# Kernel optimization log

Hardware: AMD Instinct MI355X
Metric: run time of the kernel (lower is better)

The kernel has to match this reference:

```python
import jax, jax.numpy as jnp
import numpy as np

N, C, H = 100000, 128, 8
D = C // H  # 16
E = 1600000
EPS = 1e-5
NEG_SLOPE = 0.2


def layer_norm(x, g, b):
    mu = jnp.mean(x, axis=-1, keepdims=True)
    var = jnp.mean(jnp.square(x - mu), axis=-1, keepdims=True)
    return (x - mu) * jax.lax.rsqrt(var + EPS) * g + b


def setup_inputs() -> dict:
    key = jax.random.key(0)
    ks = jax.random.split(key, 16)
    s = lambda fan: 1.0 / np.sqrt(fan)
    return {
        "x0": jax.random.normal(ks[0], (N, C), jnp.float32),
        "edges": jax.random.randint(ks[1], (2, E), 0, N, jnp.int64) if jax.config.jax_enable_x64 else jax.random.randint(ks[1], (2, E), 0, N, jnp.int32),
        "lin_l_w": jax.random.normal(ks[2], (C, C), jnp.float32) * s(C),
        "lin_r_w": jax.random.normal(ks[3], (C, C), jnp.float32) * s(C),
        "att": jax.random.normal(ks[4], (H, D), jnp.float32) * s(D),
        "gat_bias": jnp.zeros((C,), jnp.float32),
        "W_w": jax.random.normal(ks[5], (C, C), jnp.float32) * s(C),
        "g1": jnp.ones((C,), jnp.float32),
        "b1": jnp.zeros((C,), jnp.float32),
        "mlp_w1": jax.random.normal(ks[6], (2 * C, C), jnp.float32) * s(C),
        "mlp_b1": jnp.zeros((2 * C,), jnp.float32),
        "mlp_w2": jax.random.normal(ks[7], (C, 2 * C), jnp.float32) * s(2 * C),
        "mlp_b2": jnp.zeros((C,), jnp.float32),
        "g2": jnp.ones((C,), jnp.float32),
        "b2": jnp.zeros((C,), jnp.float32),
    }


def gatv2(x, edges, lin_l_w, lin_r_w, att, gat_bias):
    # GATv2Conv (concat=True, negative_slope=0.2, eval mode: no dropout)
    src, dst = edges[0], edges[1]
    x_l = (x @ lin_l_w.T).reshape(N, H, D)  # source transform
    x_r = (x @ lin_r_w.T).reshape(N, H, D)  # target transform
    e = jax.nn.leaky_relu(x_l[src] + x_r[dst], NEG_SLOPE)  # [E,H,D]
    logits = jnp.einsum("ehd,hd->eh", e, att)  # [E,H]
    # segment softmax over incoming edges per target node
    m = jax.ops.segment_max(logits, dst, num_segments=N)  # [N,H]
    m = jnp.where(jnp.isfinite(m), m, 0.0)
    ex = jnp.exp(logits - m[dst])
    denom = jax.ops.segment_sum(ex, dst, num_segments=N)  # [N,H]
    alpha = ex / (denom[dst] + 1e-16)  # [E,H]
    out = jax.ops.segment_sum(alpha[:, :, None] * x_l[src], dst, num_segments=N)
    return out.reshape(N, C) + gat_bias


def reference(x0, edges, lin_l_w, lin_r_w, att, gat_bias, W_w, g1, b1,
              mlp_w1, mlp_b1, mlp_w2, mlp_b2, g2, b2):
    x1 = gatv2(x0, edges, lin_l_w, lin_r_w, att, gat_bias)
    x2 = x1 @ W_w.T + x0
    x3 = layer_norm(x2, g1, b1)
    h = jax.nn.relu(x3 @ mlp_w1.T + mlp_b1)
    x4 = h @ mlp_w2.T + mlp_b2 + x3
    return layer_norm(x4, g2, b2)
```

## Files before the change

kernel.cpp:

```cpp
#include <hip/hip_runtime.h>

#define NN 100000
#define CC 128
#define HHEADS 8
#define EE 1600000
#define NB 196
#define BCAP 10240
#define BSTRIDE 16
#define P1C 3125

typedef unsigned short u16;
typedef unsigned int u32;
typedef __attribute__((ext_vector_type(8))) u16 u16x8;
typedef __attribute__((ext_vector_type(4))) u16 u16x4;
typedef __attribute__((ext_vector_type(8))) __bf16 bf16x8;
typedef __attribute__((ext_vector_type(4))) float f32x4;
typedef __attribute__((ext_vector_type(2))) float f32x2;

__device__ __forceinline__ float bf2f(u16 u) {
    union { u32 i; float f; } v; v.i = ((u32)u) << 16; return v.f;
}
__device__ __forceinline__ u16 f2bf(float f) {
    union { float f; u32 i; } v; v.f = f;
    u32 r = v.i + 0x7FFFu + ((v.i >> 16) & 1u);
    return (u16)(r >> 16);
}
__device__ __forceinline__ float fexp2(float x) {
    float r;
    asm volatile("v_exp_f32 %0, %1" : "=v"(r) : "v"(x));
    return r;
}

__device__ __forceinline__ f32x4 mfma16(u16x8 a, u16x8 b, f32x4 c) {
    return __builtin_amdgcn_mfma_f32_16x16x32_bf16(
        __builtin_bit_cast(bf16x8, a), __builtin_bit_cast(bf16x8, b), c, 0, 0, 0);
}

#define GLOAD(gp, lp) __builtin_amdgcn_global_load_lds( \
    (const __attribute__((address_space(1))) u32*)(gp), \
    (__attribute__((address_space(3))) u32*)(lp), 16, 0, 0)

__global__ __launch_bounds__(256) void k_pre(
    const int* __restrict__ src, const int* __restrict__ dst,
    int* __restrict__ bucketCnt, u32* __restrict__ bucketEdges,
    const float* __restrict__ x0, u16* __restrict__ x0b,
    const float* __restrict__ s0, const float* __restrict__ s1,
    const float* __restrict__ s2, const float* __restrict__ s3,
    const float* __restrict__ s4,
    u16* __restrict__ d0, u16* __restrict__ d1, u16* __restrict__ d2,
    u16* __restrict__ d3, u16* __restrict__ d4)
{
    const int b = blockIdx.x, tid = threadIdx.x;
    if (b < 512) {
        __shared__ u32 s_src[P1C];
        __shared__ u32 s_dst[P1C];
        __shared__ u32 hist[256], ssum[256], bstart[256], base[256], seq[256];
        const int beg = b * P1C;

        hist[tid] = 0; seq[tid] = 0;
        __syncthreads();

        int es[13], ds[13];
#pragma unroll
        for (int j = 0; j < 13; j++) {
            int o = tid + j * 256;
            if (o < P1C) { es[j] = src[beg + o]; ds[j] = dst[beg + o]; }
            else { es[j] = -1; ds[j] = 0; }
        }
#pragma unroll
        for (int j = 0; j < 13; j++)
            if (es[j] >= 0) atomicAdd(&hist[(u32)ds[j] >> 9], 1u);
        __syncthreads();

        u32 h = hist[tid];
        ssum[tid] = h;
        __syncthreads();
        for (int o = 1; o < 256; o <<= 1) {
            u32 v = ssum[tid];
            u32 a = (tid >= o) ? ssum[tid - o] : 0;
            __syncthreads();
            ssum[tid] = v + a;
            __syncthreads();
        }
        bstart[tid] = ssum[tid] - h;
        if (tid < NB) base[tid] = h ? (u32)atomicAdd(&bucketCnt[tid * BSTRIDE], (int)h) : 0u;
        __syncthreads();

#pragma unroll
        for (int j = 0; j < 13; j++) {
            if (es[j] >= 0) {
                u32 bb = (u32)ds[j] >> 9;
                u32 r = atomicAdd(&seq[bb], 1u);
                u32 pos = bstart[bb] + r;
                s_src[pos] = (u32)es[j];
                s_dst[pos] = (u32)ds[j];
            }
        }
        __syncthreads();

        for (int i = tid; i < P1C; i += 256) {
            u32 d = s_dst[i];
            u32 bb = d >> 9;
            u32 go = base[bb] + ((u32)i - bstart[bb]);
            if (go < BCAP)
                bucketEdges[(size_t)bb * BCAP + go] = s_src[i] | ((d & 511u) << 17);
        }
    } else if (b < 2560) {
        const int n = NN * CC;
        const int stride = 2048 * 256 * 4;
        for (int i = ((b - 512) * 256 + tid) * 4; i < n; i += stride) {
            float4 v = *(const float4*)(x0 + i);
            u16x4 o;
            o.x = f2bf(v.x); o.y = f2bf(v.y); o.z = f2bf(v.z); o.w = f2bf(v.w);
            *(u16x4*)(x0b + i) = o;
        }
    } else {
        int wb = b - 2560;
        const float* s; u16* d; int boff;
        if (wb < 16)      { s = s0; d = d0; boff = wb; }
        else if (wb < 32) { s = s1; d = d1; boff = wb - 16; }
        else if (wb < 48) { s = s2; d = d2; boff = wb - 32; }
        else if (wb < 80) { s = s3; d = d3; boff = wb - 48; }
        else              { s = s4; d = d4; boff = wb - 80; }
        int i = boff * 1024 + tid * 4;
        float4 v = *(const float4*)(s + i);
        u16x4 o;
        o.x = f2bf(v.x); o.y = f2bf(v.y); o.z = f2bf(v.z); o.w = f2bf(v.w);
        *(u16x4*)(d + i) = o;
    }
}

__global__ __launch_bounds__(256) void k_p2(const int* __restrict__ bucketCnt,
                                            u32* __restrict__ bucketEdges,
                                            int* __restrict__ offs,
                                            int* __restrict__ cnt)
{
    __shared__ u32 ebuf[BCAP];
    __shared__ u32 ncnt[512], loff[512], ssum[256];
    const int b = blockIdx.x, tid = threadIdx.x;
    int n = bucketCnt[b * BSTRIDE]; n = n < BCAP ? n : BCAP;
    u32* be = bucketEdges + (size_t)b * BCAP;

    for (int i = tid; i < n; i += 256) ebuf[i] = be[i];
    ncnt[tid] = 0; ncnt[tid + 256] = 0;
    __syncthreads();
    for (int i = tid; i < n; i += 256) atomicAdd(&ncnt[(ebuf[i] >> 17) & 511], 1u);
    __syncthreads();

    u32 a0 = ncnt[2 * tid], a1 = ncnt[2 * tid + 1];
    ssum[tid] = a0 + a1;
    __syncthreads();
    for (int o = 1; o < 256; o <<= 1) {
        u32 v = ssum[tid];
        u32 add = (tid >= o) ? ssum[tid - o] : 0;
        __syncthreads();
        ssum[tid] = v + add;
        __syncthreads();
    }
    u32 excl = ssum[tid] - (a0 + a1);
    loff[2 * tid] = excl;
    loff[2 * tid + 1] = excl + a0;

    int node0 = b * 512 + 2 * tid;
    if (node0 < NN)     { offs[node0]     = b * BCAP + (int)excl;            cnt[node0]     = (int)a0; }
    if (node0 + 1 < NN) { offs[node0 + 1] = b * BCAP + (int)(excl + a0);     cnt[node0 + 1] = (int)a1; }

    ncnt[tid] = 0; ncnt[tid + 256] = 0;
    __syncthreads();
    for (int i = tid; i < n; i += 256) {
        u32 e = ebuf[i];
        u32 ln = (e >> 17) & 511;
        u32 r = atomicAdd(&ncnt[ln], 1u);
        be[loff[ln] + r] = e & 0x1FFFFu;
    }
}

template<int K, bool BIAS, bool RELU, bool RESIDB, bool LNF>
__global__ __launch_bounds__(256, 4) void k_gemm(
    const u16* __restrict__ A, const u16* __restrict__ B,
    const float* __restrict__ bias, const u16* __restrict__ residb,
    const float* __restrict__ g, const float* __restrict__ bln,
    float* __restrict__ outf, u16* __restrict__ outb, int M, int NC)
{
    __shared__ __align__(16) u16 As[128 * 64];
    __shared__ __align__(16) u16 Bs[128 * 64];
    __shared__ float lsum[2][128], lsq[2][128];

    const int tid = threadIdx.x;
    const int lane = tid & 63;
    const int w = tid >> 6;
    const int wr = w >> 1, wc = w & 1;
    const int row0 = blockIdx.x * 128;
    const int col0 = blockIdx.y * 128;
    f32x4 acc[4][4] = {};

    for (int kt = 0; kt < K; kt += 64) {
#pragma unroll
        for (int i = 0; i < 4; i++) {
            int c = i * 256 + tid;
            int r = c >> 3;
            int kc = (c & 7) * 8;
            int ar = row0 + r; ar = ar < M ? ar : M - 1;
            GLOAD(A + (size_t)ar * K + kt + kc, As + r * 64 + kc);
            GLOAD(B + (size_t)(col0 + r) * K + kt + kc, Bs + r * 64 + kc);
        }
        asm volatile("s_waitcnt vmcnt(0)" ::: "memory");
        __syncthreads();
#pragma unroll
        for (int kk = 0; kk < 2; kk++) {
            const int ko = kk * 32 + (lane >> 4) * 8;
            u16x8 af[4], bfr[4];
#pragma unroll
            for (int m = 0; m < 4; m++)
                af[m] = *(const u16x8*)(As + (wr * 64 + m * 16 + (lane & 15)) * 64 + ko);
#pragma unroll
            for (int n = 0; n < 4; n++)
                bfr[n] = *(const u16x8*)(Bs + (wc * 64 + n * 16 + (lane & 15)) * 64 + ko);
#pragma unroll
            for (int m = 0; m < 4; m++)
#pragma unroll
                for (int n = 0; n < 4; n++)
                    acc[m][n] = mfma16(af[m], bfr[n], acc[m][n]);
        }
        __syncthreads();
    }

    const int rbase = wr * 64 + ((lane >> 4) << 2);
    const int cbase = wc * 64 + (lane & 15);

    if constexpr (!LNF) {
#pragma unroll
        for (int m = 0; m < 4; m++) {
#pragma unroll
            for (int j = 0; j < 4; j++) {
                int gr = row0 + rbase + m * 16 + j;
                if (gr < M) {
                    size_t rowoff = (size_t)gr * NC;
#pragma unroll
                    for (int n = 0; n < 4; n++) {
                        int gc = col0 + cbase + n * 16;
                        float v = acc[m][n][j];
                        if constexpr (BIAS)  v += bias[gc];
                        if constexpr (RELU)  v = fmaxf(v, 0.f);
                        if (outf) outf[rowoff + gc] = v;
                        if (outb) outb[rowoff + gc] = f2bf(v);
                    }
                }
            }
        }
    } else {
        float gv[4], bv[4];
#pragma unroll
        for (int n = 0; n < 4; n++) { gv[n] = g[cbase + n * 16]; bv[n] = bln[cbase + n * 16]; }
#pragma unroll
        for (int m = 0; m < 4; m++) {
#pragma unroll
            for (int j = 0; j < 4; j++) {
                int lr = rbase + m * 16 + j;
                int gr = row0 + lr; gr = gr < M ? gr : M - 1;
                float s = 0.f, q = 0.f;
#pragma unroll
                for (int n = 0; n < 4; n++) {
                    float v = acc[m][n][j];
                    if constexpr (BIAS)   v += bias[cbase + n * 16];
                    if constexpr (RESIDB) v += bf2f(residb[(size_t)gr * 128 + cbase + n * 16]);
                    if constexpr (RELU)   v = fmaxf(v, 0.f);
                    acc[m][n][j] = v;
                    s += v; q += v * v;
                }
                s += __shfl_xor(s, 1, 16); q += __shfl_xor(q, 1, 16);
                s += __shfl_xor(s, 2, 16); q += __shfl_xor(q, 2, 16);
                s += __shfl_xor(s, 4, 16); q += __shfl_xor(q, 4, 16);
                s += __shfl_xor(s, 8, 16); q += __shfl_xor(q, 8, 16);
                if ((lane & 15) == 0) { lsum[wc][lr] = s; lsq[wc][lr] = q; }
            }
        }
        __syncthreads();
#pragma unroll
        for (int m = 0; m < 4; m++) {
#pragma unroll
            for (int j = 0; j < 4; j++) {
                int lr = rbase + m * 16 + j;
                int gr = row0 + lr;
                if (gr < M) {
                    float s = lsum[0][lr] + lsum[1][lr];
                    float q = lsq[0][lr] + lsq[1][lr];
                    float mu = s * (1.f / 128.f);
                    float var = q * (1.f / 128.f) - mu * mu;
                    float rs = rsqrtf(var + 1e-5f);
                    size_t rowoff = (size_t)gr * 128;
#pragma unroll
                    for (int n = 0; n < 4; n++) {
                        float y = fmaf((acc[m][n][j] - mu) * rs, gv[n], bv[n]);
                        int gc = cbase + n * 16;
                        if (outf) outf[rowoff + gc] = y;
                        if (outb) outb[rowoff + gc] = f2bf(y);
                    }
                }
            }
        }
    }
}

__global__ __launch_bounds__(256, 2) void k_mlp(
    const u16* __restrict__ x3b, const u16* __restrict__ W1,
    const float* __restrict__ mb1, const u16* __restrict__ W2,
    const float* __restrict__ mb2, const float* __restrict__ g2,
    const float* __restrict__ b2, float* __restrict__ out, int M)
{
    __shared__ __align__(16) u16 x3s[128 * 128];
    __shared__ __align__(16) u16 hs[128 * 130];
    __shared__ float lsum[2][128], lsq[2][128];

    const int tid = threadIdx.x;
    const int lane = tid & 63;
    const int w = tid >> 6;
    const int wr = w >> 1, wc = w & 1;
    const int row0 = blockIdx.x * 128;
    const int rbase = wr * 64 + ((lane >> 4) << 2);
    const int cbase = wc * 64 + (lane & 15);

#pragma unroll
    for (int i = 0; i < 8; i++) {
        int c = i * 256 + tid;
        int r = c >> 4;
        int kc = (c & 15) * 8;
        int ar = row0 + r; ar = ar < M ? ar : M - 1;
        GLOAD(x3b + (size_t)ar * 128 + kc, x3s + r * 128 + kc);
    }
    asm volatile("s_waitcnt vmcnt(0)" ::: "memory");
    __syncthreads();

    f32x4 accB[4][4] = {};
    for (int half = 0; half < 2; half++) {
        f32x4 accA[4][4] = {};
#pragma unroll
        for (int kk = 0; kk < 4; kk++) {
            const int ko = kk * 32 + (lane >> 4) * 8;
            u16x8 af[4], bfr[4];
#pragma unroll
            for (int m = 0; m < 4; m++)
                af[m] = *(const u16x8*)(x3s + (wr * 64 + m * 16 + (lane & 15)) * 128 + ko);
#pragma unroll
            for (int n = 0; n < 4; n++)
                bfr[n] = *(const u16x8*)(W1 + (size_t)(half * 128 + wc * 64 + n * 16 + (lane & 15)) * 128 + ko);
#pragma unroll
            for (int m = 0; m < 4; m++)
#pragma unroll
                for (int n = 0; n < 4; n++)
                    accA[m][n] = mfma16(af[m], bfr[n], accA[m][n]);
        }
        float bv[4];
#pragma unroll
        for (int n = 0; n < 4; n++) bv[n] = mb1[half * 128 + cbase + n * 16];
#pragma unroll
        for (int m = 0; m < 4; m++)
#pragma unroll
            for (int n = 0; n < 4; n++) {
                int lc = cbase + n * 16;
#pragma unroll
                for (int j = 0; j < 4; j++) {
                    float v = fmaxf(accA[m][n][j] + bv[n], 0.f);
                    hs[(rbase + m * 16 + j) * 130 + lc] = f2bf(v);
                }
            }
        __syncthreads();

#pragma unroll
        for (int kk = 0; kk < 4; kk++) {
            const int ko = kk * 32 + (lane >> 4) * 8;
            u16x8 af[4], bfr[4];
#pragma unroll
            for (int m = 0; m < 4; m++)
                af[m] = *(const u16x8*)(hs + (wr * 64 + m * 16 + (lane & 15)) * 130 + ko);
#pragma unroll
            for (int n = 0; n < 4; n++)
                bfr[n] = *(const u16x8*)(W2 + (size_t)(wc * 64 + n * 16 + (lane & 15)) * 256 + half * 128 + ko);
#pragma unroll
            for (int m = 0; m < 4; m++)
#pragma unroll
                for (int n = 0; n < 4; n++)
                    accB[m][n] = mfma16(af[m], bfr[n], accB[m][n]);
        }
        __syncthreads();
    }

    float gv[4], bvln[4], bv2[4];
#pragma unroll
    for (int n = 0; n < 4; n++) {
        gv[n] = g2[cbase + n * 16];
        bvln[n] = b2[cbase + n * 16];
        bv2[n] = mb2[cbase + n * 16];
    }
#pragma unroll
    for (int m = 0; m < 4; m++) {
#pragma unroll
        for (int j = 0; j < 4; j++) {
            int lr = rbase + m * 16 + j;
            float s = 0.f, q = 0.f;
#pragma unroll
            for (int n = 0; n < 4; n++) {
                float v = accB[m][n][j] + bv2[n] + bf2f(x3s[lr * 128 + cbase + n * 16]);
                accB[m][n][j] = v;
                s += v; q += v * v;
            }
            s += __shfl_xor(s, 1, 16); q += __shfl_xor(q, 1, 16);
            s += __shfl_xor(s, 2, 16); q += __shfl_xor(q, 2, 16);
            s += __shfl_xor(s, 4, 16); q += __shfl_xor(q, 4, 16);
            s += __shfl_xor(s, 8, 16); q += __shfl_xor(q, 8, 16);
            if ((lane & 15) == 0) { lsum[wc][lr] = s; lsq[wc][lr] = q; }
        }
    }
    __syncthreads();
#pragma unroll
    for (int m = 0; m < 4; m++) {
#pragma unroll
        for (int j = 0; j < 4; j++) {
            int lr = rbase + m * 16 + j;
            int gr = row0 + lr;
            if (gr < M) {
                float s = lsum[0][lr] + lsum[1][lr];
                float q = lsq[0][lr] + lsq[1][lr];
                float mu = s * (1.f / 128.f);
                float var = q * (1.f / 128.f) - mu * mu;
                float rs = rsqrtf(var + 1e-5f);
                size_t rowoff = (size_t)gr * 128;
#pragma unroll
                for (int n = 0; n < 4; n++)
                    out[rowoff + cbase + n * 16] =
                        fmaf((accB[m][n][j] - mu) * rs, gv[n], bvln[n]);
            }
        }
    }
}

__global__ __launch_bounds__(256) void k_gat(const u16* __restrict__ xlr,
                                             const u32* __restrict__ csr,
                                             const int* __restrict__ offs,
                                             const int* __restrict__ cnt,
                                             const float* __restrict__ att,
                                             const float* __restrict__ gbias,
                                             u16* __restrict__ x1b)
{
    const int node = blockIdx.x * 4 + (threadIdx.x >> 6);
    const int lane = threadIdx.x & 63;
    const int slot = lane >> 4;
    const int sub  = lane & 15;
    const int c0   = sub * 8;
    const float L2E = 1.44269504f;

    f32x4 alo = *(const f32x4*)(att + c0);
    f32x4 ahi = *(const f32x4*)(att + c0 + 4);
    f32x2 av[4];
    av[0] = f32x2{alo[0], alo[1]} * L2E; av[1] = f32x2{alo[2], alo[3]} * L2E;
    av[2] = f32x2{ahi[0], ahi[1]} * L2E; av[3] = f32x2{ahi[2], ahi[3]} * L2E;

    u16x8 xr8 = *(const u16x8*)(xlr + (size_t)node * 256 + 128 + c0);
    f32x2 xrv[4];
#pragma unroll
    for (int j = 0; j < 4; j++) xrv[j] = f32x2{bf2f(xr8[2 * j]), bf2f(xr8[2 * j + 1])};

    const int beg = offs[node];
    const int deg = cnt[node];
    const int ng = (deg + 3) >> 2;

    float s = 0.f;
    f32x2 accv[4] = {};

    u16x8 xgA = {}, xgB = {};
    int ixC = 0;
    if (deg > 0) {
        int dm1 = deg - 1;
        int e0 = slot      < dm1 ? slot      : dm1;
        int e1 = slot + 4  < dm1 ? slot + 4  : dm1;
        int e2 = slot + 8  < dm1 ? slot + 8  : dm1;
        int i0 = (int)csr[beg + e0];
        int i1 = (int)csr[beg + e1];
        ixC    = (int)csr[beg + e2];
        xgA = *(const u16x8*)(xlr + (size_t)i0 * 256 + c0);
        xgB = *(const u16x8*)(xlr + (size_t)i1 * 256 + c0);
    }

    for (int g = 0; g < ng; g++) {
        u16x8 cur = xgA;
        xgA = xgB;
        xgB = *(const u16x8*)(xlr + (size_t)ixC * 256 + c0);
        int en = 4 * (g + 3) + slot; en = en < deg - 1 ? en : deg - 1;
        ixC = (int)csr[beg + (en > 0 ? en : 0)];

        const int e = 4 * g + slot;
        f32x2 xlv[4];
        f32x2 dot = {0.f, 0.f};
#pragma unroll
        for (int j = 0; j < 4; j++) {
            f32x2 xl = f32x2{bf2f(cur[2 * j]), bf2f(cur[2 * j + 1])};
            xlv[j] = xl;
            f32x2 t = xl + xrv[j];
            f32x2 t2 = t * 0.2f;
            f32x2 lr = f32x2{fmaxf(t.x, t2.x), fmaxf(t.y, t2.y)};
            dot += av[j] * lr;
        }
        float p = dot.x + dot.y;
        p += __shfl_xor(p, 1);
        float wgt = (e < deg) ? fexp2(p) : 0.f;
        s += wgt;
#pragma unroll
        for (int j = 0; j < 4; j++) accv[j] += xlv[j] * wgt;
    }

    s += __shfl_xor(s, 16);
    s += __shfl_xor(s, 32);
#pragma unroll
    for (int j = 0; j < 4; j++) {
        accv[j].x += __shfl_xor(accv[j].x, 16);
        accv[j].y += __shfl_xor(accv[j].y, 16);
        accv[j].x += __shfl_xor(accv[j].x, 32);
        accv[j].y += __shfl_xor(accv[j].y, 32);
    }

    if (slot == 0) {
        float inv = 1.f / (s + 1e-16f);
        u16x8 o;
#pragma unroll
        for (int j = 0; j < 4; j++) {
            o[2 * j]     = f2bf(fmaf(accv[j].x, inv, gbias[c0 + 2 * j]));
            o[2 * j + 1] = f2bf(fmaf(accv[j].y, inv, gbias[c0 + 2 * j + 1]));
        }
        *(u16x8*)(x1b + (size_t)node * CC + c0) = o;
    }
}

extern "C" void kernel_launch(void* const* d_in, const int* in_sizes, int n_in,
                              void* d_out, int out_size, void* d_ws, size_t ws_size,
                              hipStream_t stream) {
    const float* x0    = (const float*)d_in[0];
    const int*   edges = (const int*)d_in[1];
    const float* lin_l = (const float*)d_in[2];
    const float* lin_r = (const float*)d_in[3];
    const float* att   = (const float*)d_in[4];
    const float* gbias = (const float*)d_in[5];
    const float* Ww    = (const float*)d_in[6];
    const float* g1    = (const float*)d_in[7];
    const float* b1    = (const float*)d_in[8];
    const float* w1    = (const float*)d_in[9];
    const float* mb1   = (const float*)d_in[10];
    const float* w2    = (const float*)d_in[11];
    const float* mb2   = (const float*)d_in[12];
    const float* g2    = (const float*)d_in[13];
    const float* b2    = (const float*)d_in[14];
    float* out = (float*)d_out;

    char* ws = (char*)d_ws;
    size_t off = 0;
    auto alloc = [&](size_t bytes) {
        char* p = ws + off;
        off += (bytes + 255) & ~(size_t)255;
        return p;
    };
    u16*   x0b   = (u16*)alloc((size_t)NN * CC * 2);
    u16*   xlr   = (u16*)alloc((size_t)NN * 256 * 2);
    u16*   x1b   = (u16*)alloc((size_t)NN * CC * 2);
    u16*   Wa    = (u16*)alloc(256 * 128 * 2);
    u16*   Wb    = (u16*)alloc(128 * 128 * 2);
    u16*   W1    = (u16*)alloc(256 * 128 * 2);
    u16*   W2    = (u16*)alloc(128 * 256 * 2);
    int*   bucketCnt   = (int*)alloc((size_t)NB * BSTRIDE * 4);
    u32*   bucketEdges = (u32*)alloc((size_t)NB * BCAP * 4);
    int*   offsA       = (int*)alloc((size_t)NN * 4);
    int*   cntA        = (int*)alloc((size_t)NN * 4);
    u16*   x3b = x0b;
    (void)in_sizes; (void)n_in; (void)out_size; (void)ws_size;

    hipMemsetAsync(bucketCnt, 0, (size_t)NB * BSTRIDE * 4, stream);
    k_pre<<<2672, 256, 0, stream>>>(edges, edges + EE, bucketCnt, bucketEdges,
                                    x0, x0b, lin_l, lin_r, Ww, w1, w2,
                                    Wa, Wa + 16384, Wb, W1, W2);

    k_p2<<<NB, 256, 0, stream>>>(bucketCnt, bucketEdges, offsA, cntA);

    k_gemm<128, false, false, false, false><<<dim3(782, 2), 256, 0, stream>>>(
        x0b, Wa, nullptr, nullptr, nullptr, nullptr, nullptr, xlr, NN, 256);

    k_gat<<<NN / 4, 256, 0, stream>>>(xlr, bucketEdges, offsA, cntA, att, gbias, x1b);

    k_gemm<128, false, false, true, true><<<dim3(782, 1), 256, 0, stream>>>(
        x1b, Wb, nullptr, x0b, g1, b1, nullptr, x3b, NN, 128);

    k_mlp<<<782, 256, 0, stream>>>(x3b, W1, mb1, W2, mb2, g2, b2, out, NN);
}
```

Baseline: 214.1 us.

## Split xl/xr into separate buffers and deepen GAT gather prefetch

```diff
diff --git a/kernel.cpp b/kernel.cpp
--- a/kernel.cpp
+++ b/kernel.cpp
@@ -175,12 +175,13 @@
     }
 }
 
-template<int K, bool BIAS, bool RELU, bool RESIDB, bool LNF>
+template<int K, bool BIAS, bool RELU, bool RESIDB, bool LNF, bool SPLIT>
 __global__ __launch_bounds__(256, 4) void k_gemm(
     const u16* __restrict__ A, const u16* __restrict__ B,
     const float* __restrict__ bias, const u16* __restrict__ residb,
     const float* __restrict__ g, const float* __restrict__ bln,
-    float* __restrict__ outf, u16* __restrict__ outb, int M, int NC)
+    float* __restrict__ outf, u16* __restrict__ outb, u16* __restrict__ outbB,
+    int M, int NC)
 {
     __shared__ __align__(16) u16 As[128 * 64];
     __shared__ __align__(16) u16 Bs[128 * 64];
@@ -229,6 +230,8 @@
     const int cbase = wc * 64 + (lane & 15);
 
     if constexpr (!LNF) {
+        u16* ob = outb;
+        if constexpr (SPLIT) ob = col0 ? outbB : outb;
 #pragma unroll
         for (int m = 0; m < 4; m++) {
 #pragma unroll
@@ -238,12 +241,12 @@
                     size_t rowoff = (size_t)gr * NC;
 #pragma unroll
                     for (int n = 0; n < 4; n++) {
-                        int gc = col0 + cbase + n * 16;
+                        int gc = (SPLIT ? 0 : col0) + cbase + n * 16;
                         float v = acc[m][n][j];
-                        if constexpr (BIAS)  v += bias[gc];
+                        if constexpr (BIAS)  v += bias[col0 + cbase + n * 16];
                         if constexpr (RELU)  v = fmaxf(v, 0.f);
                         if (outf) outf[rowoff + gc] = v;
-                        if (outb) outb[rowoff + gc] = f2bf(v);
+                        if (ob) ob[rowoff + gc] = f2bf(v);
                     }
                 }
             }
@@ -434,7 +437,8 @@
     }
 }
 
-__global__ __launch_bounds__(256) void k_gat(const u16* __restrict__ xlr,
+__global__ __launch_bounds__(256) void k_gat(const u16* __restrict__ xlb,
+                                             const u16* __restrict__ xrb,
                                              const u32* __restrict__ csr,
                                              const int* __restrict__ offs,
                                              const int* __restrict__ cnt,
@@ -455,7 +459,7 @@
     av[0] = f32x2{alo[0], alo[1]} * L2E; av[1] = f32x2{alo[2], alo[3]} * L2E;
     av[2] = f32x2{ahi[0], ahi[1]} * L2E; av[3] = f32x2{ahi[2], ahi[3]} * L2E;
 
-    u16x8 xr8 = *(const u16x8*)(xlr + (size_t)node * 256 + 128 + c0);
+    u16x8 xr8 = *(const u16x8*)(xrb + (size_t)node * 128 + c0);
     f32x2 xrv[4];
 #pragma unroll
     for (int j = 0; j < 4; j++) xrv[j] = f32x2{bf2f(xr8[2 * j]), bf2f(xr8[2 * j + 1])};
@@ -463,30 +467,35 @@
     const int beg = offs[node];
     const int deg = cnt[node];
     const int ng = (deg + 3) >> 2;
+    const int dm1 = deg - 1;
+
+    auto idxof = [&](int gi) -> int {
+        if (gi >= ng) return 0;
+        int en = 4 * gi + slot; en = en < dm1 ? en : dm1;
+        return (int)csr[beg + en];
+    };
+    auto rowld = [&](int ix) -> u16x8 {
+        return *(const u16x8*)(xlb + (size_t)ix * 128 + c0);
+    };
 
     float s = 0.f;
     f32x2 accv[4] = {};
 
-    u16x8 xgA = {}, xgB = {};
-    int ixC = 0;
+    u16x8 xgA = {}, xgB = {}, xgC = {};
+    int ixD = 0;
     if (deg > 0) {
-        int dm1 = deg - 1;
-        int e0 = slot      < dm1 ? slot      : dm1;
-        int e1 = slot + 4  < dm1 ? slot + 4  : dm1;
-        int e2 = slot + 8  < dm1 ? slot + 8  : dm1;
-        int i0 = (int)csr[beg + e0];
-        int i1 = (int)csr[beg + e1];
-        ixC    = (int)csr[beg + e2];
-        xgA = *(const u16x8*)(xlr + (size_t)i0 * 256 + c0);
-        xgB = *(const u16x8*)(xlr + (size_t)i1 * 256 + c0);
+        xgA = rowld(idxof(0));
+        xgB = rowld(idxof(1));
+        xgC = rowld(idxof(2));
+        ixD = idxof(3);
     }
 
     for (int g = 0; g < ng; g++) {
         u16x8 cur = xgA;
         xgA = xgB;
-        xgB = *(const u16x8*)(xlr + (size_t)ixC * 256 + c0);
-        int en = 4 * (g + 3) + slot; en = en < deg - 1 ? en : deg - 1;
-        ixC = (int)csr[beg + (en > 0 ? en : 0)];
+        xgB = xgC;
+        xgC = rowld(ixD);
+        ixD = idxof(g + 4);
 
         const int e = 4 * g + slot;
         f32x2 xlv[4];
@@ -558,7 +567,8 @@
         return p;
     };
     u16*   x0b   = (u16*)alloc((size_t)NN * CC * 2);
-    u16*   xlr   = (u16*)alloc((size_t)NN * 256 * 2);
+    u16*   xlb   = (u16*)alloc((size_t)NN * 128 * 2);
+    u16*   xrb   = (u16*)alloc((size_t)NN * 128 * 2);
     u16*   x1b   = (u16*)alloc((size_t)NN * CC * 2);
     u16*   Wa    = (u16*)alloc(256 * 128 * 2);
     u16*   Wb    = (u16*)alloc(128 * 128 * 2);
@@ -578,13 +588,13 @@
 
     k_p2<<<NB, 256, 0, stream>>>(bucketCnt, bucketEdges, offsA, cntA);
 
-    k_gemm<128, false, false, false, false><<<dim3(782, 2), 256, 0, stream>>>(
-        x0b, Wa, nullptr, nullptr, nullptr, nullptr, nullptr, xlr, NN, 256);
-
-    k_gat<<<NN / 4, 256, 0, stream>>>(xlr, bucketEdges, offsA, cntA, att, gbias, x1b);
-
-    k_gemm<128, false, false, true, true><<<dim3(782, 1), 256, 0, stream>>>(
-        x1b, Wb, nullptr, x0b, g1, b1, nullptr, x3b, NN, 128);
+    k_gemm<128, false, false, false, false, true><<<dim3(782, 2), 256, 0, stream>>>(
+        x0b, Wa, nullptr, nullptr, nullptr, nullptr, nullptr, xlb, xrb, NN, 128);
+
+    k_gat<<<NN / 4, 256, 0, stream>>>(xlb, xrb, bucketEdges, offsA, cntA, att, gbias, x1b);
+
+    k_gemm<128, false, false, true, true, false><<<dim3(782, 1), 256, 0, stream>>>(
+        x1b, Wb, nullptr, x0b, g1, b1, nullptr, x3b, nullptr, NN, 128);
 
     k_mlp<<<782, 256, 0, stream>>>(x3b, W1, mb1, W2, mb2, g2, b2, out, NN);
 }
```

Measured after the change: 224.0 us. 4.6% more time.

## Fuse W projection, residual, LayerNorm1 and MLP into one tail kernel

Applied to the files above, without the earlier changes.

```diff
diff --git a/kernel.cpp b/kernel.cpp
--- a/kernel.cpp
+++ b/kernel.cpp
@@ -175,16 +175,13 @@
     }
 }
 
-template<int K, bool BIAS, bool RELU, bool RESIDB, bool LNF>
+template<int K>
 __global__ __launch_bounds__(256, 4) void k_gemm(
     const u16* __restrict__ A, const u16* __restrict__ B,
-    const float* __restrict__ bias, const u16* __restrict__ residb,
-    const float* __restrict__ g, const float* __restrict__ bln,
-    float* __restrict__ outf, u16* __restrict__ outb, int M, int NC)
+    u16* __restrict__ outb, int M, int NC)
 {
     __shared__ __align__(16) u16 As[128 * 64];
     __shared__ __align__(16) u16 Bs[128 * 64];
-    __shared__ float lsum[2][128], lsq[2][128];
 
     const int tid = threadIdx.x;
     const int lane = tid & 63;
@@ -227,89 +224,33 @@
 
     const int rbase = wr * 64 + ((lane >> 4) << 2);
     const int cbase = wc * 64 + (lane & 15);
-
-    if constexpr (!LNF) {
-#pragma unroll
-        for (int m = 0; m < 4; m++) {
-#pragma unroll
-            for (int j = 0; j < 4; j++) {
-                int gr = row0 + rbase + m * 16 + j;
-                if (gr < M) {
-                    size_t rowoff = (size_t)gr * NC;
-#pragma unroll
-                    for (int n = 0; n < 4; n++) {
-                        int gc = col0 + cbase + n * 16;
-                        float v = acc[m][n][j];
-                        if constexpr (BIAS)  v += bias[gc];
-                        if constexpr (RELU)  v = fmaxf(v, 0.f);
-                        if (outf) outf[rowoff + gc] = v;
-                        if (outb) outb[rowoff + gc] = f2bf(v);
-                    }
+#pragma unroll
+    for (int m = 0; m < 4; m++) {
+#pragma unroll
+        for (int j = 0; j < 4; j++) {
+            int gr = row0 + rbase + m * 16 + j;
+            if (gr < M) {
+                size_t rowoff = (size_t)gr * NC;
+#pragma unroll
+                for (int n = 0; n < 4; n++) {
+                    int gc = col0 + cbase + n * 16;
+                    outb[rowoff + gc] = f2bf(acc[m][n][j]);
                 }
             }
         }
-    } else {
-        float gv[4], bv[4];
-#pragma unroll
-        for (int n = 0; n < 4; n++) { gv[n] = g[cbase + n * 16]; bv[n] = bln[cbase + n * 16]; }
-#pragma unroll
-        for (int m = 0; m < 4; m++) {
-#pragma unroll
-            for (int j = 0; j < 4; j++) {
-                int lr = rbase + m * 16 + j;
-                int gr = row0 + lr; gr = gr < M ? gr : M - 1;
-                float s = 0.f, q = 0.f;
-#pragma unroll
-                for (int n = 0; n < 4; n++) {
-                    float v = acc[m][n][j];
-                    if constexpr (BIAS)   v += bias[cbase + n * 16];
-                    if constexpr (RESIDB) v += bf2f(residb[(size_t)gr * 128 + cbase + n * 16]);
-                    if constexpr (RELU)   v = fmaxf(v, 0.f);
-                    acc[m][n][j] = v;
-                    s += v; q += v * v;
-                }
-                s += __shfl_xor(s, 1, 16); q += __shfl_xor(q, 1, 16);
-                s += __shfl_xor(s, 2, 16); q += __shfl_xor(q, 2, 16);
-                s += __shfl_xor(s, 4, 16); q += __shfl_xor(q, 4, 16);
-                s += __shfl_xor(s, 8, 16); q += __shfl_xor(q, 8, 16);
-                if ((lane & 15) == 0) { lsum[wc][lr] = s; lsq[wc][lr] = q; }
-            }
-        }
-        __syncthreads();
-#pragma unroll
-        for (int m = 0; m < 4; m++) {
-#pragma unroll
-            for (int j = 0; j < 4; j++) {
-                int lr = rbase + m * 16 + j;
-                int gr = row0 + lr;
-                if (gr < M) {
-                    float s = lsum[0][lr] + lsum[1][lr];
-                    float q = lsq[0][lr] + lsq[1][lr];
-                    float mu = s * (1.f / 128.f);
-                    float var = q * (1.f / 128.f) - mu * mu;
-                    float rs = rsqrtf(var + 1e-5f);
-                    size_t rowoff = (size_t)gr * 128;
-#pragma unroll
-                    for (int n = 0; n < 4; n++) {
-                        float y = fmaf((acc[m][n][j] - mu) * rs, gv[n], bv[n]);
-                        int gc = cbase + n * 16;
-                        if (outf) outf[rowoff + gc] = y;
-                        if (outb) outb[rowoff + gc] = f2bf(y);
-                    }
-                }
-            }
-        }
-    }
-}
-
-__global__ __launch_bounds__(256, 2) void k_mlp(
-    const u16* __restrict__ x3b, const u16* __restrict__ W1,
+    }
+}
+
+__global__ __launch_bounds__(256, 2) void k_tail(
+    const u16* __restrict__ x1b, const u16* __restrict__ Wb,
+    const u16* __restrict__ x0b, const float* __restrict__ g1,
+    const float* __restrict__ b1, const u16* __restrict__ W1,
     const float* __restrict__ mb1, const u16* __restrict__ W2,
     const float* __restrict__ mb2, const float* __restrict__ g2,
     const float* __restrict__ b2, float* __restrict__ out, int M)
 {
-    __shared__ __align__(16) u16 x3s[128 * 128];
-    __shared__ __align__(16) u16 hs[128 * 130];
+    __shared__ __align__(16) u16 bufA[128 * 128];
+    __shared__ __align__(16) u16 bufB[128 * 130];
     __shared__ float lsum[2][128], lsq[2][128];
 
     const int tid = threadIdx.x;
@@ -326,9 +267,72 @@
         int r = c >> 4;
         int kc = (c & 15) * 8;
         int ar = row0 + r; ar = ar < M ? ar : M - 1;
-        GLOAD(x3b + (size_t)ar * 128 + kc, x3s + r * 128 + kc);
+        GLOAD(x1b + (size_t)ar * 128 + kc, bufA + r * 128 + kc);
+        GLOAD(x0b + (size_t)ar * 128 + kc, bufB + r * 128 + kc);
     }
     asm volatile("s_waitcnt vmcnt(0)" ::: "memory");
+    __syncthreads();
+
+    f32x4 accW[4][4] = {};
+#pragma unroll
+    for (int kk = 0; kk < 4; kk++) {
+        const int ko = kk * 32 + (lane >> 4) * 8;
+        u16x8 af[4], bfr[4];
+#pragma unroll
+        for (int m = 0; m < 4; m++)
+            af[m] = *(const u16x8*)(bufA + (wr * 64 + m * 16 + (lane & 15)) * 128 + ko);
+#pragma unroll
+        for (int n = 0; n < 4; n++)
+            bfr[n] = *(const u16x8*)(Wb + (size_t)(wc * 64 + n * 16 + (lane & 15)) * 128 + ko);
+#pragma unroll
+        for (int m = 0; m < 4; m++)
+#pragma unroll
+            for (int n = 0; n < 4; n++)
+                accW[m][n] = mfma16(af[m], bfr[n], accW[m][n]);
+    }
+
+#pragma unroll
+    for (int m = 0; m < 4; m++) {
+#pragma unroll
+        for (int j = 0; j < 4; j++) {
+            int lr = rbase + m * 16 + j;
+            float s = 0.f, q = 0.f;
+#pragma unroll
+            for (int n = 0; n < 4; n++) {
+                float v = accW[m][n][j] + bf2f(bufB[lr * 128 + cbase + n * 16]);
+                accW[m][n][j] = v;
+                s += v; q += v * v;
+            }
+            s += __shfl_xor(s, 1, 16); q += __shfl_xor(q, 1, 16);
+            s += __shfl_xor(s, 2, 16); q += __shfl_xor(q, 2, 16);
+            s += __shfl_xor(s, 4, 16); q += __shfl_xor(q, 4, 16);
+            s += __shfl_xor(s, 8, 16); q += __shfl_xor(q, 8, 16);
+            if ((lane & 15) == 0) { lsum[wc][lr] = s; lsq[wc][lr] = q; }
+        }
+    }
+    __syncthreads();
+
+    {
+        float gv[4], bv[4];
+#pragma unroll
+        for (int n = 0; n < 4; n++) { gv[n] = g1[cbase + n * 16]; bv[n] = b1[cbase + n * 16]; }
+#pragma unroll
+        for (int m = 0; m < 4; m++) {
+#pragma unroll
+            for (int j = 0; j < 4; j++) {
+                int lr = rbase + m * 16 + j;
+                float s = lsum[0][lr] + lsum[1][lr];
+                float q = lsq[0][lr] + lsq[1][lr];
+                float mu = s * (1.f / 128.f);
+                float var = q * (1.f / 128.f) - mu * mu;
+                float rs = rsqrtf(var + 1e-5f);
+#pragma unroll
+                for (int n = 0; n < 4; n++)
+                    bufA[lr * 128 + cbase + n * 16] =
+                        f2bf(fmaf((accW[m][n][j] - mu) * rs, gv[n], bv[n]));
+            }
+        }
+    }
     __syncthreads();
 
     f32x4 accB[4][4] = {};
@@ -340,7 +344,7 @@
             u16x8 af[4], bfr[4];
 #pragma unroll
             for (int m = 0; m < 4; m++)
-                af[m] = *(const u16x8*)(x3s + (wr * 64 + m * 16 + (lane & 15)) * 128 + ko);
+                af[m] = *(const u16x8*)(bufA + (wr * 64 + m * 16 + (lane & 15)) * 128 + ko);
 #pragma unroll
             for (int n = 0; n < 4; n++)
                 bfr[n] = *(const u16x8*)(W1 + (size_t)(half * 128 + wc * 64 + n * 16 + (lane & 15)) * 128 + ko);
@@ -361,7 +365,7 @@
 #pragma unroll
                 for (int j = 0; j < 4; j++) {
                     float v = fmaxf(accA[m][n][j] + bv[n], 0.f);
-                    hs[(rbase + m * 16 + j) * 130 + lc] = f2bf(v);
+                    bufB[(rbase + m * 16 + j) * 130 + lc] = f2bf(v);
                 }
             }
         __syncthreads();
@@ -372,7 +376,7 @@
             u16x8 af[4], bfr[4];
 #pragma unroll
             for (int m = 0; m < 4; m++)
-                af[m] = *(const u16x8*)(hs + (wr * 64 + m * 16 + (lane & 15)) * 130 + ko);
+                af[m] = *(const u16x8*)(bufB + (wr * 64 + m * 16 + (lane & 15)) * 130 + ko);
 #pragma unroll
             for (int n = 0; n < 4; n++)
                 bfr[n] = *(const u16x8*)(W2 + (size_t)(wc * 64 + n * 16 + (lane & 15)) * 256 + half * 128 + ko);
@@ -400,7 +404,7 @@
             float s = 0.f, q = 0.f;
 #pragma unroll
             for (int n = 0; n < 4; n++) {
-                float v = accB[m][n][j] + bv2[n] + bf2f(x3s[lr * 128 + cbase + n * 16]);
+                float v = accB[m][n][j] + bv2[n] + bf2f(bufA[lr * 128 + cbase + n * 16]);
                 accB[m][n][j] = v;
                 s += v; q += v * v;
             }
@@ -568,7 +572,6 @@
     u32*   bucketEdges = (u32*)alloc((size_t)NB * BCAP * 4);
     int*   offsA       = (int*)alloc((size_t)NN * 4);
     int*   cntA        = (int*)alloc((size_t)NN * 4);
-    u16*   x3b = x0b;
     (void)in_sizes; (void)n_in; (void)out_size; (void)ws_size;
 
     hipMemsetAsync(bucketCnt, 0, (size_t)NB * BSTRIDE * 4, stream);
@@ -578,13 +581,10 @@
 
     k_p2<<<NB, 256, 0, stream>>>(bucketCnt, bucketEdges, offsA, cntA);
 
-    k_gemm<128, false, false, false, false><<<dim3(782, 2), 256, 0, stream>>>(
-        x0b, Wa, nullptr, nullptr, nullptr, nullptr, nullptr, xlr, NN, 256);
+    k_gemm<128><<<dim3(782, 2), 256, 0, stream>>>(x0b, Wa, xlr, NN, 256);
 
     k_gat<<<NN / 4, 256, 0, stream>>>(xlr, bucketEdges, offsA, cntA, att, gbias, x1b);
 
-    k_gemm<128, false, false, true, true><<<dim3(782, 1), 256, 0, stream>>>(
-        x1b, Wb, nullptr, x0b, g1, b1, nullptr, x3b, NN, 128);
-
-    k_mlp<<<782, 256, 0, stream>>>(x3b, W1, mb1, W2, mb2, g2, b2, out, NN);
-}
+    k_tail<<<782, 256, 0, stream>>>(x1b, Wb, x0b, g1, b1, W1, mb1, W2, mb2,
+                                    g2, b2, out, NN);
+}
```

Measured after the change: 211.8 us. About the same (-1.1%).
